# Kernel optimization log

Measured on AMD Instinct MI355X. Metric: run time of the kernel, lower is better.

Reference implementation:

```python
import jax, jax.numpy as jnp
import numpy as np
import math

B, S, D, H = 4, 2048, 1024, 16
DK = D // H

def setup_inputs() -> dict:
    key = jax.random.key(0)
    ks = jax.random.split(key, 11)
    mk = lambda k, shape: jax.random.normal(k, shape, dtype=jnp.float32)
    inp = {
        'query': mk(ks[0], (B, S, D)),
        'key':   mk(ks[1], (B, S, D)),
        'value': mk(ks[2], (B, S, D)),
        'Wq': mk(ks[3], (D, D)) * 0.02, 'bq': jnp.zeros((D,), jnp.float32),
        'Wk': mk(ks[4], (D, D)) * 0.02, 'bk': jnp.zeros((D,), jnp.float32),
        'Wv': mk(ks[5], (D, D)) * 0.02, 'bv': jnp.zeros((D,), jnp.float32),
        'Wo': mk(ks[6], (D, D)) * 0.02, 'bo': jnp.zeros((D,), jnp.float32),
    }
    return inp

def reference(query, key, value, Wq, bq, Wk, bk, Wv, bv, Wo, bo):
    b, s, d = query.shape
    scale = 1.0 / math.sqrt(DK)
    def proj(x, W, bias):
        # nn.Linear: x @ W.T + b, then split heads -> [b, h, s, dk]
        return (x @ W.T + bias).reshape(b, s, H, DK).transpose(0, 2, 1, 3)
    q = proj(query, Wq, bq)
    k = proj(key, Wk, bk)
    v = proj(value, Wv, bv)
    scores = jnp.einsum('bhqd,bhkd->bhqk', q, k) * scale  # [b,h,s,s]
    attn = jax.nn.softmax(scores, axis=-1)
    # dropout is identity in eval/reference mode
    x = jnp.einsum('bhqk,bhkd->bhqd', attn, v)
    x = x.transpose(0, 2, 1, 3).reshape(b, s, d)
    return x @ Wo.T + bo
```

## Files before the change

kernel.cpp:

```cpp
#include <hip/hip_runtime.h>
#include <stdint.h>

#define DEV static __device__ __forceinline__

typedef __bf16 bf16_t;
typedef bf16_t bf16x8 __attribute__((ext_vector_type(8)));
typedef bf16_t bf16x4 __attribute__((ext_vector_type(4)));
typedef float f32x4 __attribute__((ext_vector_type(4)));

static constexpr int Bc = 4, Sc = 2048, Dc = 1024, Hc = 16, DKc = 64;
static constexpr int Mrows = Bc * Sc;

DEV unsigned short f2bf(float f) {
  unsigned int u = __float_as_uint(f);
  u += 0x7fffu + ((u >> 16) & 1u);
  return (unsigned short)(u >> 16);
}

DEV float fexp2(float x) {
#if __has_builtin(__builtin_amdgcn_exp2f)
  return __builtin_amdgcn_exp2f(x);
#else
  return exp2f(x);
#endif
}

#if __has_builtin(__builtin_amdgcn_mfma_f32_16x16x16_bf16)
DEV f32x4 mfma16(bf16x4 a, bf16x4 b, f32x4 c) {
  return __builtin_amdgcn_mfma_f32_16x16x16_bf16(a, b, c, 0, 0, 0);
}
#elif __has_builtin(__builtin_amdgcn_mfma_f32_16x16x16bf16_1k)
typedef short s16x4 __attribute__((ext_vector_type(4)));
DEV f32x4 mfma16(bf16x4 a, bf16x4 b, f32x4 c) {
  union U { bf16x4 h; s16x4 s; };
  U ua, ub; ua.h = a; ub.h = b;
  return __builtin_amdgcn_mfma_f32_16x16x16bf16_1k(ua.s, ub.s, c, 0, 0, 0);
}
#else
DEV f32x4 mfma16(bf16x4 a, bf16x4 b, f32x4 c) {
  asm("v_mfma_f32_16x16x16_bf16 %0, %1, %2, %0" : "+v"(c) : "v"(a), "v"(b));
  return c;
}
#endif

DEV void gload_lds16(const void* g, void* l) {
  __builtin_amdgcn_global_load_lds(
      (const __attribute__((address_space(1))) void*)g,
      (__attribute__((address_space(3))) void*)l, 16, 0, 0);
}

DEV bf16x8 cvt8(float4 a, float4 b) {
  bf16x8 r;
  r[0] = (bf16_t)a.x; r[1] = (bf16_t)a.y; r[2] = (bf16_t)a.z; r[3] = (bf16_t)a.w;
  r[4] = (bf16_t)b.x; r[5] = (bf16_t)b.y; r[6] = (bf16_t)b.z; r[7] = (bf16_t)b.w;
  return r;
}

__global__ void __launch_bounds__(256) cvt_bf16_seg_kernel(
    const float* __restrict__ s0, const float* __restrict__ s1,
    const float* __restrict__ s2, const float* __restrict__ s3,
    unsigned short* __restrict__ out, int lg) {
  int i = blockIdx.x * blockDim.x + threadIdx.x;
  int seg = i >> lg, j = i & ((1 << lg) - 1);
  const float* src = seg == 0 ? s0 : seg == 1 ? s1 : seg == 2 ? s2 : s3;
  float4 v = reinterpret_cast<const float4*>(src)[j];
  ushort4 o;
  o.x = f2bf(v.x); o.y = f2bf(v.y); o.z = f2bf(v.z); o.w = f2bf(v.w);
  reinterpret_cast<ushort4*>(out)[i] = o;
}

template <bool QKV>
__global__ void __launch_bounds__(256) gemm_dbuf_kernel(
    const void* __restrict__ A0v, const void* __restrict__ A1v,
    const void* __restrict__ A2v,
    const unsigned short* __restrict__ W0, const unsigned short* __restrict__ W1,
    const unsigned short* __restrict__ W2,
    const float* __restrict__ b0, const float* __restrict__ b1,
    const float* __restrict__ b2,
    void* __restrict__ C0, void* __restrict__ C1, void* __restrict__ C2,
    int M, int N, int K, float scale0) {
  __shared__ unsigned short lA[3][128 * 32];
  __shared__ unsigned short lB[3][128 * 32];
  const int t = threadIdx.x;
  const int wv = t >> 6, ln = t & 63;
  const int l15 = ln & 15, lhi = ln >> 4;

  const void* Av; const unsigned short* W;
  const float* bias; void* Cout; float scale; int mode;
  if (QKV) {
    const int z = blockIdx.z;
    Av = z == 0 ? A0v : z == 1 ? A1v : A2v;
    W = z == 0 ? W0 : z == 1 ? W1 : W2;
    bias = z == 0 ? b0 : z == 1 ? b1 : b2;
    Cout = z == 0 ? C0 : z == 1 ? C1 : C2;
    scale = z == 0 ? scale0 : 1.0f;
    mode = z == 2 ? 2 : 1;
  } else {
    Av = A0v; W = W0; bias = b0; Cout = C0; scale = scale0; mode = 0;
  }

  const int nwg = gridDim.x * gridDim.y;
  const int hw = blockIdx.y * gridDim.x + blockIdx.x;
  const int chunk = nwg >> 3;
  const int swzid = (hw & 7) * chunk + (hw >> 3);
  const int m0 = (swzid / gridDim.x) * 128, n0 = (swzid % gridDim.x) * 128;
  const int wr = wv >> 1, wc = wv & 1;
  const int swzR = (l15 & 3) << 4;

  const int rowA = t >> 2;
  const int colS = ((t & 3) ^ (rowA & 3)) * 8;
  const unsigned short* wS = W + (size_t)(n0 + rowA) * K + colS;
  const size_t rstep = (size_t)64 * K;
  const int d0 = t * 16, d1 = 4096 + t * 16;
  const float* aF = QKV ? (const float*)Av + (size_t)(m0 + rowA) * K + colS : nullptr;
  const unsigned short* aB =
      QKV ? nullptr : (const unsigned short*)Av + (size_t)(m0 + rowA) * K + colS;

  f32x4 acc[4][4] = {};
  const int NK = K >> 5;

#define WST(bi, k0_)                                           \
  do {                                                         \
    gload_lds16(wS + (k0_), (char*)lB[bi] + d0);               \
    gload_lds16(wS + rstep + (k0_), (char*)lB[bi] + d1);       \
  } while (0)

#define MFMA_BLOCK(cur_)                                                        \
  do {                                                                          \
    bf16x8 af[4], bfr[4];                                                       \
    _Pragma("unroll") for (int i = 0; i < 4; ++i)                               \
      af[i] = *reinterpret_cast<const bf16x8*>(                                 \
          (char*)lA[cur_] + (((wr * 64 + i * 16 + l15) * 64 + lhi * 16) ^ swzR));\
    _Pragma("unroll") for (int j = 0; j < 4; ++j)                               \
      bfr[j] = *reinterpret_cast<const bf16x8*>(                                \
          (char*)lB[cur_] + (((wc * 64 + j * 16 + l15) * 64 + lhi * 16) ^ swzR));\
    _Pragma("unroll") for (int i = 0; i < 4; ++i)                               \
      _Pragma("unroll") for (int j = 0; j < 4; ++j)                             \
        acc[i][j] = __builtin_amdgcn_mfma_f32_16x16x32_bf16(af[i], bfr[j],      \
                                                            acc[i][j], 0, 0, 0);\
  } while (0)

  if (QKV) {
    float4 a0, a1, a2, a3;
    float4 n0_, n1_, n2_, n3_;
#define ALD(k0_)                                               \
  do {                                                         \
    const float* p = aF + (k0_);                               \
    a0 = *(const float4*)(p);     a1 = *(const float4*)(p + 4);\
    a2 = *(const float4*)(p + rstep); a3 = *(const float4*)(p + rstep + 4);\
  } while (0)
#define ALDN(k0_)                                              \
  do {                                                         \
    const float* p = aF + (k0_);                               \
    n0_ = *(const float4*)(p);     n1_ = *(const float4*)(p + 4);\
    n2_ = *(const float4*)(p + rstep); n3_ = *(const float4*)(p + rstep + 4);\
  } while (0)
#define AWR(bi)                                                \
  do {                                                         \
    *reinterpret_cast<bf16x8*>((char*)lA[bi] + d0) = cvt8(a0, a1);\
    *reinterpret_cast<bf16x8*>((char*)lA[bi] + d1) = cvt8(a2, a3);\
  } while (0)
    WST(0, 0);
    ALD(0);
    AWR(0);
    WST(1, 32);
    ALD(32);
    asm volatile("s_waitcnt vmcnt(6) lgkmcnt(0)" ::: "memory");
    __builtin_amdgcn_s_barrier();
    __builtin_amdgcn_sched_barrier(0);

    for (int tk = 0; tk < NK; ++tk) {
      const int cur = tk % 3;
      const bool hn = (tk + 1 < NK), hn2 = (tk + 2 < NK);
      if (hn2) {
        WST((tk + 2) % 3, (tk + 2) * 32);
        ALDN((tk + 2) * 32);
      }
      __builtin_amdgcn_sched_barrier(0);
      MFMA_BLOCK(cur);
      if (hn) AWR((tk + 1) % 3);
      if (hn2) { a0 = n0_; a1 = n1_; a2 = n2_; a3 = n3_; }
      if (hn2)
        asm volatile("s_waitcnt vmcnt(6) lgkmcnt(0)" ::: "memory");
      else
        asm volatile("s_waitcnt vmcnt(0) lgkmcnt(0)" ::: "memory");
      __builtin_amdgcn_s_barrier();
      __builtin_amdgcn_sched_barrier(0);
    }
#undef ALD
#undef ALDN
#undef AWR
  } else {
#define AST(bi, k0_)                                           \
  do {                                                         \
    gload_lds16(aB + (k0_), (char*)lA[bi] + d0);               \
    gload_lds16(aB + rstep + (k0_), (char*)lA[bi] + d1);       \
  } while (0)
    AST(0, 0); WST(0, 0);
    AST(1, 32); WST(1, 32);
    for (int tk = 0; tk < NK; ++tk) {
      const int cur = tk % 3;
      if (tk == NK - 1)
        asm volatile("s_waitcnt vmcnt(0)" ::: "memory");
      else
        asm volatile("s_waitcnt vmcnt(4)" ::: "memory");
      __builtin_amdgcn_s_barrier();
      __builtin_amdgcn_sched_barrier(0);
      if (tk + 2 < NK) {
        AST((tk + 2) % 3, (tk + 2) * 32);
        WST((tk + 2) % 3, (tk + 2) * 32);
      }
      MFMA_BLOCK(cur);
    }
#undef AST
  }
#undef WST
#undef MFMA_BLOCK

#pragma unroll
  for (int i = 0; i < 4; ++i)
#pragma unroll
    for (int j = 0; j < 4; ++j) {
      int n = n0 + wc * 64 + j * 16 + l15;
      float bv = bias[n];
      if (QKV && mode == 2) {
        int mb = m0 + wr * 64 + i * 16 + lhi * 4;
        int sl = mb & (Sc - 1);
        int pl = (sl & ~60) | ((sl & 48) >> 2) | ((sl & 12) << 2);
        ushort4 ov;
        ov.x = f2bf((acc[i][j][0] + bv) * scale);
        ov.y = f2bf((acc[i][j][1] + bv) * scale);
        ov.z = f2bf((acc[i][j][2] + bv) * scale);
        ov.w = f2bf((acc[i][j][3] + bv) * scale);
        *reinterpret_cast<ushort4*>((unsigned short*)Cout +
            ((size_t)(mb >> 11) * Dc + n) * Sc + pl) = ov;
      } else {
#pragma unroll
        for (int jj = 0; jj < 4; ++jj) {
          int m = m0 + wr * 64 + i * 16 + lhi * 4 + jj;
          float v = (acc[i][j][jj] + bv) * scale;
          if (QKV)
            ((unsigned short*)Cout)[(size_t)m * N + n] = f2bf(v);
          else
            ((float*)Cout)[(size_t)m * N + n] = v;
        }
      }
    }
}

__global__ void __launch_bounds__(512, 4) attn_kernel(
    const unsigned short* __restrict__ Q, const unsigned short* __restrict__ Kk,
    const unsigned short* __restrict__ Vt, unsigned short* __restrict__ X) {
  __shared__ unsigned short lK[2][128 * 64];
  __shared__ unsigned short lVT[2][64 * 128];
  const int t = threadIdx.x;
  const int wv = t >> 6, ln = t & 63;
  const int l15 = ln & 15, lhi = ln >> 4;
  const int q0 = blockIdx.x * 128;
  const int h = blockIdx.y, b = blockIdx.z;
  const size_t base = (size_t)b * Sc * Dc;
  const int hoff = h * DKc;

  bf16x8 qf[2];
  {
    const unsigned short* qp = Q + base + (size_t)(q0 + wv * 16 + l15) * Dc + hoff + lhi * 8;
    qf[0] = *reinterpret_cast<const bf16x8*>(qp);
    qf[1] = *reinterpret_cast<const bf16x8*>(qp + 32);
  }

  const int kvr = t >> 3;
  const int kcol = ((t & 7) * 8) ^ ((kvr & 7) << 3);
  const unsigned short* kS = Kk + base + (size_t)kvr * Dc + hoff + kcol;
  const int vdk = t >> 4;
  const int vkv = ((t & 15) * 8) ^ ((vdk & 7) << 3);
  const unsigned short* vS = Vt + ((size_t)b * Dc + hoff + vdk) * Sc + vkv;

  f32x4 xacc[4] = {};
  f32x4 lsum = {};
  const int swzK = (l15 & 7) << 4;

  bf16x4 ones4;
#pragma unroll
  for (int i = 0; i < 4; ++i) ones4[i] = (bf16_t)1.0f;

#define DSTAGE(bi, kv0_)                                                        \
  do {                                                                          \
    gload_lds16(kS + (size_t)(kv0_)*Dc, (char*)lK[bi] + t * 16);                \
    gload_lds16(kS + (size_t)((kv0_) + 64) * Dc, (char*)lK[bi] + 8192 + t * 16);\
    gload_lds16(vS + (kv0_), (char*)lVT[bi] + t * 16);                          \
    gload_lds16(vS + (size_t)32 * Sc + (kv0_), (char*)lVT[bi] + 8192 + t * 16); \
  } while (0)

  DSTAGE(0, 0);
  asm volatile("s_waitcnt vmcnt(0)" ::: "memory");
  __builtin_amdgcn_s_barrier();
  __builtin_amdgcn_sched_barrier(0);

  const int NT2 = Sc / 128;
  for (int tt = 0; tt < NT2; ++tt) {
    const int cur = tt & 1;
    if (tt + 1 < NT2) DSTAGE(cur ^ 1, (tt + 1) * 128);

    const char* K_ = (const char*)lK[cur];
    const char* VT_ = (const char*)lVT[cur];

    f32x4 sacc[2][4];
    __builtin_amdgcn_s_setprio(1);
#pragma unroll
    for (int s64 = 0; s64 < 2; ++s64)
#pragma unroll
      for (int ct = 0; ct < 4; ++ct) {
        f32x4 z = {};
#pragma unroll
        for (int kk = 0; kk < 2; ++kk) {
          bf16x8 kf = *reinterpret_cast<const bf16x8*>(
              K_ + (((s64 * 64 + ct * 16 + l15) * 128 + kk * 64 + lhi * 16) ^ swzK));
          z = __builtin_amdgcn_mfma_f32_16x16x32_bf16(kf, qf[kk], z, 0, 0, 0);
        }
        sacc[s64][ct] = z;
      }
    __builtin_amdgcn_s_setprio(0);

    __builtin_amdgcn_s_setprio(1);
#pragma unroll
    for (int s64 = 0; s64 < 2; ++s64) {
      bf16x4 pa[4];
#pragma unroll
      for (int ct = 0; ct < 4; ++ct)
#pragma unroll
        for (int jj = 0; jj < 4; ++jj)
          pa[ct][jj] = (bf16_t)fexp2(sacc[s64][ct][jj]);
#pragma unroll
      for (int ct = 0; ct < 4; ++ct) lsum = mfma16(pa[ct], ones4, lsum);
#pragma unroll
      for (int dt = 0; dt < 4; ++dt) {
#pragma unroll
        for (int sel = 0; sel < 2; ++sel) {
          bf16x8 vb2 = *reinterpret_cast<const bf16x8*>(
              VT_ + (((dt * 16 + l15) * 256 + s64 * 128 + lhi * 32 + sel * 16) ^ swzK));
          bf16x4 vlo = __builtin_shufflevector(vb2, vb2, 0, 1, 2, 3);
          bf16x4 vhi = __builtin_shufflevector(vb2, vb2, 4, 5, 6, 7);
          xacc[dt] = mfma16(pa[2 * sel + 0], vlo, xacc[dt]);
          xacc[dt] = mfma16(pa[2 * sel + 1], vhi, xacc[dt]);
        }
      }
    }
    __builtin_amdgcn_s_setprio(0);

    asm volatile("s_waitcnt vmcnt(0)" ::: "memory");
    __builtin_amdgcn_s_barrier();
    __builtin_amdgcn_sched_barrier(0);
  }
#undef DSTAGE

  float iO[4];
#pragma unroll
  for (int jj = 0; jj < 4; ++jj) iO[jj] = 1.0f / lsum[jj];

  unsigned short* xp = X + base + (size_t)(q0 + wv * 16) * Dc + hoff;
#pragma unroll
  for (int dt = 0; dt < 4; ++dt)
#pragma unroll
    for (int jj = 0; jj < 4; ++jj) {
      int r = lhi * 4 + jj;
      xp[(size_t)r * Dc + dt * 16 + l15] = f2bf(xacc[dt][jj] * iO[jj]);
    }
}

extern "C" void kernel_launch(void* const* d_in, const int* in_sizes, int n_in,
                              void* d_out, int out_size, void* d_ws, size_t ws_size,
                              hipStream_t stream) {
  const float* query = (const float*)d_in[0];
  const float* key   = (const float*)d_in[1];
  const float* value = (const float*)d_in[2];
  const float* Wq = (const float*)d_in[3];
  const float* bq = (const float*)d_in[4];
  const float* Wk = (const float*)d_in[5];
  const float* bk = (const float*)d_in[6];
  const float* Wv = (const float*)d_in[7];
  const float* bv = (const float*)d_in[8];
  const float* Wo = (const float*)d_in[9];
  const float* bo = (const float*)d_in[10];

  const size_t NBS = (size_t)Mrows * Dc;
  const size_t NW  = (size_t)Dc * Dc;
  unsigned short* bWq  = (unsigned short*)d_ws;
  unsigned short* bWk  = bWq + NW;
  unsigned short* bWv  = bWk + NW;
  unsigned short* bWo  = bWv + NW;
  unsigned short* Qp   = bWo + NW;
  unsigned short* Kp   = Qp + NBS;
  unsigned short* Vtp  = Kp + NBS;
  unsigned short* Xp   = Vtp + NBS;

  cvt_bf16_seg_kernel<<<(int)(4 * NW / 1024), 256, 0, stream>>>(
      Wq, Wk, Wv, Wo, bWq, 18);

  gemm_dbuf_kernel<true><<<dim3(Dc / 128, Mrows / 128, 3), 256, 0, stream>>>(
      query, key, value, bWq, bWk, bWv, bq, bk, bv, Qp, Kp, Vtp,
      Mrows, Dc, Dc, 0.125f * 1.44269504088896340736f);

  attn_kernel<<<dim3(Sc / 128, Hc, Bc), 512, 0, stream>>>(Qp, Kp, Vtp, Xp);

  gemm_dbuf_kernel<false><<<dim3(Dc / 128, Mrows / 128, 1), 256, 0, stream>>>(
      Xp, nullptr, nullptr, bWo, nullptr, nullptr, bo, nullptr, nullptr,
      d_out, nullptr, nullptr, Mrows, Dc, Dc, 1.0f);
}
```

Baseline: 215.2 us.

## Process two query subtiles per wave and remap attention blocks for XCD locality

Each attention block now covers 256 queries, with each wave handling two 16-row query subtiles. Every K and V fragment read from LDS is therefore reused across two MFMA streams, which halves LDS traffic and K/V global loads per query. The exp and row-sum work is interleaved per column tile instead of run as separate phases, which shortens the lifetime of the score registers. Block indices are also remapped so blocks sharing a (batch, head) are grouped, presumably for L2 or XCD locality. In exchange, per-thread register use goes up and the grid has half as many blocks, which may lower occupancy or leave compute units less evenly loaded.

```diff
diff --git a/kernel.cpp b/kernel.cpp
--- a/kernel.cpp
+++ b/kernel.cpp
@@ -256,16 +256,21 @@
   const int t = threadIdx.x;
   const int wv = t >> 6, ln = t & 63;
   const int l15 = ln & 15, lhi = ln >> 4;
-  const int q0 = blockIdx.x * 128;
-  const int h = blockIdx.y, b = blockIdx.z;
+  const int lin = blockIdx.x + (blockIdx.y << 3) + (blockIdx.z << 7);
+  const int jb = lin >> 3;
+  const int p = (lin & 7) * 8 + (jb >> 3);
+  const int q0 = (jb & 7) * 256;
+  const int h = p & 15, b = p >> 4;
   const size_t base = (size_t)b * Sc * Dc;
   const int hoff = h * DKc;
 
-  bf16x8 qf[2];
-  {
-    const unsigned short* qp = Q + base + (size_t)(q0 + wv * 16 + l15) * Dc + hoff + lhi * 8;
-    qf[0] = *reinterpret_cast<const bf16x8*>(qp);
-    qf[1] = *reinterpret_cast<const bf16x8*>(qp + 32);
+  bf16x8 qf[2][2];
+#pragma unroll
+  for (int s = 0; s < 2; ++s) {
+    const unsigned short* qp =
+        Q + base + (size_t)(q0 + wv * 32 + s * 16 + l15) * Dc + hoff + lhi * 8;
+    qf[s][0] = *reinterpret_cast<const bf16x8*>(qp);
+    qf[s][1] = *reinterpret_cast<const bf16x8*>(qp + 32);
   }
 
   const int kvr = t >> 3;
@@ -275,8 +280,8 @@
   const int vkv = ((t & 15) * 8) ^ ((vdk & 7) << 3);
   const unsigned short* vS = Vt + ((size_t)b * Dc + hoff + vdk) * Sc + vkv;
 
-  f32x4 xacc[4] = {};
-  f32x4 lsum = {};
+  f32x4 xacc[2][4] = {};
+  f32x4 lsum[2] = {};
   const int swzK = (l15 & 7) << 4;
 
   bf16x4 ones4;
@@ -304,48 +309,45 @@
     const char* K_ = (const char*)lK[cur];
     const char* VT_ = (const char*)lVT[cur];
 
-    f32x4 sacc[2][4];
-    __builtin_amdgcn_s_setprio(1);
-#pragma unroll
-    for (int s64 = 0; s64 < 2; ++s64)
-#pragma unroll
-      for (int ct = 0; ct < 4; ++ct) {
-        f32x4 z = {};
-#pragma unroll
-        for (int kk = 0; kk < 2; ++kk) {
-          bf16x8 kf = *reinterpret_cast<const bf16x8*>(
-              K_ + (((s64 * 64 + ct * 16 + l15) * 128 + kk * 64 + lhi * 16) ^ swzK));
-          z = __builtin_amdgcn_mfma_f32_16x16x32_bf16(kf, qf[kk], z, 0, 0, 0);
+#pragma unroll
+    for (int s64 = 0; s64 < 2; ++s64) {
+#pragma unroll
+      for (int sel = 0; sel < 2; ++sel) {
+        bf16x4 pa[2][2];
+        __builtin_amdgcn_s_setprio(1);
+#pragma unroll
+        for (int ci = 0; ci < 2; ++ci) {
+          const int ct = sel * 2 + ci;
+          bf16x8 kf0 = *reinterpret_cast<const bf16x8*>(
+              K_ + (((s64 * 64 + ct * 16 + l15) * 128 + lhi * 16) ^ swzK));
+          bf16x8 kf1 = *reinterpret_cast<const bf16x8*>(
+              K_ + (((s64 * 64 + ct * 16 + l15) * 128 + 64 + lhi * 16) ^ swzK));
+#pragma unroll
+          for (int s = 0; s < 2; ++s) {
+            f32x4 z = {};
+            z = __builtin_amdgcn_mfma_f32_16x16x32_bf16(kf0, qf[s][0], z, 0, 0, 0);
+            z = __builtin_amdgcn_mfma_f32_16x16x32_bf16(kf1, qf[s][1], z, 0, 0, 0);
+#pragma unroll
+            for (int jj = 0; jj < 4; ++jj)
+              pa[s][ci][jj] = (bf16_t)fexp2(z[jj]);
+            lsum[s] = mfma16(pa[s][ci], ones4, lsum[s]);
+          }
         }
-        sacc[s64][ct] = z;
-      }
-    __builtin_amdgcn_s_setprio(0);
-
-    __builtin_amdgcn_s_setprio(1);
-#pragma unroll
-    for (int s64 = 0; s64 < 2; ++s64) {
-      bf16x4 pa[4];
-#pragma unroll
-      for (int ct = 0; ct < 4; ++ct)
-#pragma unroll
-        for (int jj = 0; jj < 4; ++jj)
-          pa[ct][jj] = (bf16_t)fexp2(sacc[s64][ct][jj]);
-#pragma unroll
-      for (int ct = 0; ct < 4; ++ct) lsum = mfma16(pa[ct], ones4, lsum);
-#pragma unroll
-      for (int dt = 0; dt < 4; ++dt) {
-#pragma unroll
-        for (int sel = 0; sel < 2; ++sel) {
+        __builtin_amdgcn_s_setprio(0);
+#pragma unroll
+        for (int dt = 0; dt < 4; ++dt) {
           bf16x8 vb2 = *reinterpret_cast<const bf16x8*>(
               VT_ + (((dt * 16 + l15) * 256 + s64 * 128 + lhi * 32 + sel * 16) ^ swzK));
           bf16x4 vlo = __builtin_shufflevector(vb2, vb2, 0, 1, 2, 3);
           bf16x4 vhi = __builtin_shufflevector(vb2, vb2, 4, 5, 6, 7);
-          xacc[dt] = mfma16(pa[2 * sel + 0], vlo, xacc[dt]);
-          xacc[dt] = mfma16(pa[2 * sel + 1], vhi, xacc[dt]);
+#pragma unroll
+          for (int s = 0; s < 2; ++s) {
+            xacc[s][dt] = mfma16(pa[s][0], vlo, xacc[s][dt]);
+            xacc[s][dt] = mfma16(pa[s][1], vhi, xacc[s][dt]);
+          }
         }
       }
     }
-    __builtin_amdgcn_s_setprio(0);
 
     asm volatile("s_waitcnt vmcnt(0)" ::: "memory");
     __builtin_amdgcn_s_barrier();
@@ -353,18 +355,21 @@
   }
 #undef DSTAGE
 
-  float iO[4];
-#pragma unroll
-  for (int jj = 0; jj < 4; ++jj) iO[jj] = 1.0f / lsum[jj];
-
-  unsigned short* xp = X + base + (size_t)(q0 + wv * 16) * Dc + hoff;
-#pragma unroll
-  for (int dt = 0; dt < 4; ++dt)
-#pragma unroll
-    for (int jj = 0; jj < 4; ++jj) {
-      int r = lhi * 4 + jj;
-      xp[(size_t)r * Dc + dt * 16 + l15] = f2bf(xacc[dt][jj] * iO[jj]);
-    }
+#pragma unroll
+  for (int s = 0; s < 2; ++s) {
+    float iO[4];
+#pragma unroll
+    for (int jj = 0; jj < 4; ++jj) iO[jj] = 1.0f / lsum[s][jj];
+    unsigned short* xp =
+        X + base + (size_t)(q0 + wv * 32 + s * 16) * Dc + hoff;
+#pragma unroll
+    for (int dt = 0; dt < 4; ++dt)
+#pragma unroll
+      for (int jj = 0; jj < 4; ++jj) {
+        int r = lhi * 4 + jj;
+        xp[(size_t)r * Dc + dt * 16 + l15] = f2bf(xacc[s][dt][jj] * iO[jj]);
+      }
+  }
 }
 
 extern "C" void kernel_launch(void* const* d_in, const int* in_sizes, int n_in,
@@ -400,7 +405,7 @@
       query, key, value, bWq, bWk, bWv, bq, bk, bv, Qp, Kp, Vtp,
       Mrows, Dc, Dc, 0.125f * 1.44269504088896340736f);
 
-  attn_kernel<<<dim3(Sc / 128, Hc, Bc), 512, 0, stream>>>(Qp, Kp, Vtp, Xp);
+  attn_kernel<<<dim3(Sc / 256, Hc, Bc), 512, 0, stream>>>(Qp, Kp, Vtp, Xp);
 
   gemm_dbuf_kernel<false><<<dim3(Dc / 128, Mrows / 128, 1), 256, 0, stream>>>(
       Xp, nullptr, nullptr, bWo, nullptr, nullptr, bo, nullptr, nullptr,
```

Result: faster. 195.9 us (-9.0%).
